# Optimization experiments

Measured on AMD Instinct MI355X. Metric: run time of the kernel, lower is better.

Reference implementation:

```python
import jax, jax.numpy as jnp
import numpy as np
import math

PHI = (1.0 + math.sqrt(5.0)) / 2.0
V, D, L, N, H = 50257, 128, 2, 512, 8
DH = D // H
B, S = 2, 256


def setup_inputs() -> dict:
    key = jax.random.key(0)
    ks = jax.random.split(key, 16)
    lim = 0.5 * math.sqrt(6.0 / (N + D))  # xavier_uniform gain=0.5 for Linear(N->D)
    return {
        "tokens": jax.random.randint(ks[0], (B, S), 0, V),
        "emb": (jax.random.normal(ks[1], (V, 2 * D)) * 0.02) * 0.5,
        "wq": jax.random.normal(ks[2], (L, H, DH)) * 0.02,
        "bq": jnp.zeros((L, H, DH)),
        "wk": jax.random.normal(ks[3], (L, H, DH)) * 0.02,
        "bk": jnp.zeros((L, H, DH)),
        "w_out": jax.random.normal(ks[4], (L, D)) * 0.02,
        "b_out": jnp.zeros((L, D)),
        "out_scale": jnp.ones((L, D)) * 0.5,
        "Wf": jax.random.normal(ks[5], (L, N, D)) * 0.02,
        "Bf": jnp.zeros((L, N, D)),
        "proj_real": jax.random.uniform(ks[6], (L, D, N), minval=-lim, maxval=lim),
        "proj_imag": jax.random.uniform(ks[7], (L, D, N), minval=-lim, maxval=lim),
        "attn_scale": jnp.ones((L,)),
        "res_scale": jnp.ones((L,)),
        "out_proj": jax.random.normal(ks[8], (V, D)) * 0.02,
    }


def reference(tokens, emb, wq, bq, wk, bk, w_out, b_out, out_scale, Wf, Bf,
              proj_real, proj_imag, attn_scale, res_scale, out_proj):
    dtype = emb.dtype
    wb = emb[tokens]                      # [B,S,2D] token -> (w, b) pairs
    w_e, b_e = wb[..., :D], wb[..., D:]
    t = jnp.arange(S, dtype=dtype)        # timestep per position

    # Recurrent Euler state evolution: theta = s/(1+|w|) + b + t*PHI ; s' = cos+sin
    def step(s, inp):
        w_t, b_t, tt = inp
        theta = s / (1.0 + jnp.abs(w_t)) + b_t + tt * PHI
        s_new = jnp.cos(theta) + jnp.sin(theta)
        return s_new, s_new

    _, states = jax.lax.scan(
        step, jnp.zeros((B, D), dtype),
        (jnp.moveaxis(w_e, 1, 0), jnp.moveaxis(b_e, 1, 0), t))
    states = jnp.moveaxis(states, 0, 1)   # [B,S,D] cached states

    causal = jnp.tril(jnp.ones((S, S), bool))  # cache includes current state
    t_phi = t * PHI
    scale = math.sqrt(2 * DH)

    x = states
    for l in range(L):
        # --- Euler attention ---
        xh = x.reshape(B, S, H, DH)
        th_q = xh / (1.0 + jnp.abs(wq[l])) + bq[l] + t_phi[None, :, None, None]
        q = jnp.concatenate([jnp.cos(th_q), jnp.sin(th_q)], axis=-1)  # [B,S,H,2DH]
        kh = states.reshape(B, S, H, DH)
        th_k = kh / (1.0 + jnp.abs(wk[l])) + bk[l]
        k = jnp.concatenate([jnp.cos(th_k), jnp.sin(th_k)], axis=-1)
        scores = jnp.einsum('bqhd,bkhd->bhqk', q, k) / scale
        scores = jnp.where(causal[None, None], scores, -jnp.inf)
        wts = jax.nn.softmax(scores, axis=-1)
        # each head attends over full-width cached states; heads are summed
        context = jnp.einsum('bhqk,bkd->bqd', wts, states)
        th_o = context / (1.0 + jnp.abs(w_out[l])) + b_out[l] + t_phi[None, :, None]
        attn_out = out_scale[l] * (jnp.cos(th_o) + jnp.sin(th_o))
        # --- Resonant FFN (per-neuron interference) ---
        th_f = x[:, :, None, :] / (1.0 + jnp.abs(Wf[l])) + Bf[l] + t[None, :, None, None]
        cos_sum = jnp.cos(th_f).sum(axis=-1)   # [B,S,N]
        sin_sum = jnp.sin(th_f).sum(axis=-1)
        res = cos_sum @ proj_real[l].T + sin_sum @ proj_imag[l].T
        res = jax.nn.silu(res)
        # additive fusion
        x = x + attn_scale[l] * attn_out + res_scale[l] * res

    logits = x @ out_proj.T                # [B,S,V]
    return logits
```

## Files before the change

### kernel.cpp

```cpp
#include <hip/hip_runtime.h>
#include <hip/hip_bf16.h>

using bf16x8 = __attribute__((ext_vector_type(8))) short;
using f32x4  = __attribute__((ext_vector_type(4))) float;

constexpr int cV  = 50257;
constexpr int cVp = 50688;
constexpr int cD  = 128;
constexpr int cN  = 512;
constexpr int cS  = 256;

#define PHI_F    1.6180339887498949f
#define INV2PI_F 0.15915494309189535f
#define SQRT2_F  1.4142135623730951f

__device__ __forceinline__ float fract1(float x) { return x - floorf(x); }

#if __has_builtin(__builtin_amdgcn_sinf)
__device__ __forceinline__ float sin_rev(float r) { return __builtin_amdgcn_sinf(r); }
__device__ __forceinline__ float cos_rev(float r) { return __builtin_amdgcn_cosf(r); }
#else
__device__ __forceinline__ float sin_rev(float r) { return __sinf(r * 6.2831853071795865f); }
__device__ __forceinline__ float cos_rev(float r) { return __cosf(r * 6.2831853071795865f); }
#endif

__device__ __forceinline__ unsigned short f2bf(float f) {
  unsigned u = __float_as_uint(f);
  unsigned r = (u + 0x7FFFu + ((u >> 16) & 1u)) >> 16;
  return (unsigned short)r;
}

__global__ void k_setup(const int* __restrict__ tokens, const float* __restrict__ emb,
                        float2* __restrict__ mc,
                        const float* __restrict__ pr, const float* __restrict__ pi,
                        float* __restrict__ pTR, float* __restrict__ pTI,
                        const float* __restrict__ W, unsigned short* __restrict__ Wbf) {
  int blk = blockIdx.x;
  if (blk < 256) {
    int idx = blk * 256 + threadIdx.x;
    int t = idx & 255, s = idx >> 8;
    int b = t >> 7, d = t & 127;
    int tok = tokens[b * cS + s];
    float w  = emb[tok * (2 * cD) + d];
    float be = emb[tok * (2 * cD) + cD + d];
    float m2 = SQRT2_F * INV2PI_F / (1.f + fabsf(w));
    float c  = fmaf((float)s, PHI_F, be) * INV2PI_F + 0.125f;
    mc[idx] = make_float2(m2, c);
  } else if (blk < 768) {
    int idx = (blk - 256) * 256 + threadIdx.x;
    int l = idx >> 16, rem = idx & 65535;
    int n = rem >> 7, d = rem & 127;
    int src = (l * cD + d) * cN + n;
    pTR[idx] = pr[src];
    pTI[idx] = pi[src];
  } else {
    int idx = (blk - 768) * 256 + threadIdx.x;
    int row = idx >> 4, c0 = (idx & 15) * 8;
    ushort4 o0 = {0,0,0,0}, o1 = {0,0,0,0};
    if (row < cV) {
      float4 w0 = *(const float4*)(W + (size_t)row * cD + c0);
      float4 w1 = *(const float4*)(W + (size_t)row * cD + c0 + 4);
      o0 = { f2bf(w0.x), f2bf(w0.y), f2bf(w0.z), f2bf(w0.w) };
      o1 = { f2bf(w1.x), f2bf(w1.y), f2bf(w1.z), f2bf(w1.w) };
    }
    unsigned short* dst = Wbf + (size_t)row * cD + c0;
    *(ushort4*)dst = o0;
    *(ushort4*)(dst + 4) = o1;
  }
}

__global__ void k_scan(const float2* __restrict__ mc, float* __restrict__ states) {
  int t = threadIdx.x;
  int b = t >> 7, d = t & 127;
  float2 buf[8];
#pragma unroll
  for (int i = 0; i < 8; ++i) buf[i] = mc[i * 256 + t];
  float sv = 0.f;
  float* out = states + (b * cS) * cD + d;
#pragma unroll 8
  for (int s = 0; s < cS; ++s) {
    float2 v = buf[s & 7];
    if (s + 8 < cS) buf[s & 7] = mc[(s + 8) * 256 + t];
    float r = fmaf(sv, v.x, v.y);
    sv = sin_rev(fract1(r));
    out[s * cD] = sv * SQRT2_F;
  }
}

__global__ __launch_bounds__(512) void k_layer(const float* __restrict__ x, const float* __restrict__ states,
                                               const float* __restrict__ wq, const float* __restrict__ bq,
                                               const float* __restrict__ wk, const float* __restrict__ bk,
                                               const float* __restrict__ Wf, const float* __restrict__ Bf,
                                               float* __restrict__ ctx, float* __restrict__ U, float* __restrict__ Vv) {
  int blk = blockIdx.x;
  if (blk < 256) {
    __shared__ __align__(16) float qrow[2][256];
    __shared__ float Psum[2][256];
    __shared__ float redm[2][4], reds[2][4];
    __shared__ float cred[2][256];
    __shared__ __align__(16) float rkl[128], bkl[128];
    int b = blk >> 7, qp = blk & 127;
    int sub = threadIdx.x >> 8;
    int t = threadIdx.x & 255;
    int q = qp * 2 + sub;
    if (threadIdx.x < 128) {
      int hd = threadIdx.x;
      rkl[hd] = INV2PI_F / (1.f + fabsf(wk[hd]));
      bkl[hd] = bk[hd] * INV2PI_F;
    }
    if (t < 128) {
      int hd = t;
      float rq = 1.f / (1.f + fabsf(wq[hd]));
      float thq = fmaf(x[(b * cS + q) * cD + hd], rq, fmaf((float)q, PHI_F, bq[hd])) * INV2PI_F;
      float fq = fract1(thq);
      qrow[sub][hd]       = cos_rev(fq);
      qrow[sub][128 + hd] = sin_rev(fq);
    }
    Psum[sub][t] = 0.f;
    __syncthreads();
    bool act = (t <= q);
    float sc[8];
    const float4* Sr = (const float4*)(states + (b * cS + t) * cD);
#pragma unroll
    for (int h = 0; h < 8; ++h) {
      float sacc = 0.f;
#pragma unroll
      for (int j = 0; j < 4; ++j) {
        float4 sv4 = Sr[h * 4 + j];
        int hd = h * 16 + j * 4;
        float sva[4] = { sv4.x, sv4.y, sv4.z, sv4.w };
#pragma unroll
        for (int c = 0; c < 4; ++c) {
          float f = fract1(fmaf(sva[c], rkl[hd + c], bkl[hd + c]));
          float ck = cos_rev(f), sk = sin_rev(f);
          sacc = fmaf(qrow[sub][hd + c], ck, fmaf(qrow[sub][128 + hd + c], sk, sacc));
        }
      }
      sc[h] = act ? sacc * 0.17677669529663689f : -3.0e38f;
    }
    int wid = t >> 6;
    for (int h = 0; h < 8; ++h) {
      float v = sc[h];
#pragma unroll
      for (int off = 32; off; off >>= 1) v = fmaxf(v, __shfl_xor(v, off, 64));
      if ((t & 63) == 0) redm[sub][wid] = v;
      __syncthreads();
      float m = fmaxf(fmaxf(redm[sub][0], redm[sub][1]), fmaxf(redm[sub][2], redm[sub][3]));
      float p = act ? __expf(sc[h] - m) : 0.f;
      float ps = p;
#pragma unroll
      for (int off = 32; off; off >>= 1) ps += __shfl_xor(ps, off, 64);
      if ((t & 63) == 0) reds[sub][wid] = ps;
      __syncthreads();
      float tot = reds[sub][0] + reds[sub][1] + reds[sub][2] + reds[sub][3];
      Psum[sub][t] += p / tot;
    }
    __syncthreads();
    int d = t & 127, half = t >> 7;
    float acc = 0.f;
    int k0 = half * 128;
    int kend = min(k0 + 128, q + 1);
    for (int kk = k0; kk < kend; ++kk)
      acc = fmaf(Psum[sub][kk], states[(b * cS + kk) * cD + d], acc);
    cred[sub][t] = acc;
    __syncthreads();
    if (half == 0) ctx[(b * cS + q) * cD + d] = cred[sub][t] + cred[sub][t + 128];
  } else {
    int fblk = blk - 256;
    int ns = fblk & 15, tg = fblk >> 4;
    constexpr int P = 130;
    __shared__ __align__(16) float finv[32 * P];
    __shared__ __align__(16) float fb[32 * P];
    __shared__ __align__(16) float xl[32 * 128];
    int t = threadIdx.x;
#pragma unroll
    for (int i = 0; i < 8; ++i) {
      int idx = t + i * 512;
      int rl = idx >> 7, d = idx & 127;
      int g = (ns * 32 + rl) * cD + d;
      finv[rl * P + d] = INV2PI_F / (1.f + fabsf(Wf[g]));
      fb[rl * P + d]   = Bf[g] * INV2PI_F;
      xl[idx] = x[(tg * 32 + rl) * cD + d];
    }
    __syncthreads();
    int nl = t & 31, tli = t >> 5;
#pragma unroll
    for (int p = 0; p < 2; ++p) {
      int tl = p * 16 + tli;
      int T = tg * 32 + tl;
      float srev = (float)(T & 255) * INV2PI_F;
      float uc = 0.f, us = 0.f;
      const float* fi  = finv + nl * P;
      const float* fbp = fb + nl * P;
      const float* xr  = xl + tl * 128;
#pragma unroll 4
      for (int d = 0; d < cD; d += 2) {
        float2 fiv = *(const float2*)(fi + d);
        float2 fbv = *(const float2*)(fbp + d);
        float2 xv  = *(const float2*)(xr + d);
        float f0 = fract1(fmaf(xv.x, fiv.x, fbv.x) + srev);
        float f1 = fract1(fmaf(xv.y, fiv.y, fbv.y) + srev);
        uc += cos_rev(f0);
        us += sin_rev(f0);
        uc += cos_rev(f1);
        us += sin_rev(f1);
      }
      U[T * cN + ns * 32 + nl]  = uc;
      Vv[T * cN + ns * 32 + nl] = us;
    }
  }
}

__global__ __launch_bounds__(512) void k_res(const float* __restrict__ U, const float* __restrict__ Vv,
                                             const float* __restrict__ pTR, const float* __restrict__ pTI,
                                             const float* __restrict__ ctx, const float* __restrict__ x,
                                             const float* __restrict__ w_out, const float* __restrict__ b_out,
                                             const float* __restrict__ out_scale,
                                             const float* __restrict__ attn_scale, const float* __restrict__ res_scale,
                                             int l, float* __restrict__ xout, unsigned short* __restrict__ xbf) {
  int blk = blockIdx.x;
  int t = threadIdx.x;
  __shared__ __align__(16) float uvU[4][512], uvV[4][512];
  __shared__ __align__(16) float4 part[3][4][32];
#pragma unroll
  for (int i = 0; i < 4; ++i) {
    int idx = t + i * 512;
    int tok = idx >> 9, n = idx & 511;
    uvU[tok][n] = U[(blk * 4 + tok) * cN + n];
    uvV[tok][n] = Vv[(blk * 4 + tok) * cN + n];
  }
  __syncthreads();
  int d4 = t & 31, tok = (t >> 5) & 3, nh = t >> 7;
  int T = blk * 4 + tok, s = T & 255;
  float a0 = 0.f, a1 = 0.f, a2 = 0.f, a3 = 0.f;
  const float* prB = pTR + (size_t)(l * cN) * cD + d4 * 4;
  const float* piB = pTI + (size_t)(l * cN) * cD + d4 * 4;
  int n0 = nh * 128;
#pragma unroll 4
  for (int n = n0; n < n0 + 128; ++n) {
    float4 pr = *(const float4*)(prB + n * cD);
    float4 pi = *(const float4*)(piB + n * cD);
    float wr = uvU[tok][n], wi = uvV[tok][n];
    a0 = fmaf(wr, pr.x, fmaf(wi, pi.x, a0));
    a1 = fmaf(wr, pr.y, fmaf(wi, pi.y, a1));
    a2 = fmaf(wr, pr.z, fmaf(wi, pi.z, a2));
    a3 = fmaf(wr, pr.w, fmaf(wi, pi.w, a3));
  }
  if (nh > 0) part[nh - 1][tok][d4] = make_float4(a0, a1, a2, a3);
  __syncthreads();
  if (nh == 0) {
    float rr[4] = { a0, a1, a2, a3 };
#pragma unroll
    for (int j = 0; j < 3; ++j) {
      float4 p = part[j][tok][d4];
      rr[0] += p.x; rr[1] += p.y; rr[2] += p.z; rr[3] += p.w;
    }
    int di = d4 * 4;
    float4 cx  = *(const float4*)(ctx + T * cD + di);
    float4 wo  = *(const float4*)(w_out + l * cD + di);
    float4 bo  = *(const float4*)(b_out + l * cD + di);
    float4 osc = *(const float4*)(out_scale + l * cD + di);
    float4 xv  = *(const float4*)(x + T * cD + di);
    float as = attn_scale[l], rs = res_scale[l];
    float sphi = (float)s * PHI_F;
    float cxa[4] = { cx.x, cx.y, cx.z, cx.w };
    float woa[4] = { wo.x, wo.y, wo.z, wo.w };
    float boa[4] = { bo.x, bo.y, bo.z, bo.w };
    float osa[4] = { osc.x, osc.y, osc.z, osc.w };
    float xva[4] = { xv.x, xv.y, xv.z, xv.w };
    float oa[4];
#pragma unroll
    for (int c = 0; c < 4; ++c) {
      float th = fmaf(cxa[c], 1.f / (1.f + fabsf(woa[c])), boa[c]) + sphi;
      float f = fract1(th * INV2PI_F);
      float ao = osa[c] * (cos_rev(f) + sin_rev(f));
      float r = rr[c];
      float sil = r / (1.f + __expf(-r));
      oa[c] = fmaf(as, ao, fmaf(rs, sil, xva[c]));
    }
    *(float4*)(xout + T * cD + di) = make_float4(oa[0], oa[1], oa[2], oa[3]);
    if (xbf) {
      ushort4 b4 = { f2bf(oa[0]), f2bf(oa[1]), f2bf(oa[2]), f2bf(oa[3]) };
      *(ushort4*)(xbf + T * cD + di) = b4;
    }
  }
}

__global__ __launch_bounds__(256) void k_gemm(const unsigned short* __restrict__ Xbf,
                                              const unsigned short* __restrict__ Wbf,
                                              float* __restrict__ out) {
  __shared__ __align__(16) float Cst[4][16 * 132];
  int t = threadIdx.x;
  int mchunk = blockIdx.x / 99, vchunk = blockIdx.x % 99;
  int m0 = mchunk * 64;
  int v0 = vchunk * 512;
  int wid = t >> 6, lane = t & 63, lr = lane & 15, lk = lane >> 4;
  int wv = wid * 128;
  const bf16x8* Xp = (const bf16x8*)Xbf;
  const bf16x8* Wp = (const bf16x8*)Wbf;
  f32x4 acc[4][8];
#pragma unroll
  for (int fm = 0; fm < 4; ++fm)
#pragma unroll
    for (int fv = 0; fv < 8; ++fv) acc[fm][fv] = (f32x4){0.f, 0.f, 0.f, 0.f};
#pragma unroll
  for (int ks = 0; ks < 4; ++ks) {
    bf16x8 a[4];
#pragma unroll
    for (int fm = 0; fm < 4; ++fm)
      a[fm] = Xp[(m0 + fm * 16 + lr) * 16 + ks * 4 + lk];
#pragma unroll
    for (int fv = 0; fv < 8; ++fv) {
      bf16x8 b = Wp[(size_t)(v0 + wv + fv * 16 + lr) * 16 + ks * 4 + lk];
#pragma unroll
      for (int fm = 0; fm < 4; ++fm)
        acc[fm][fv] = __builtin_amdgcn_mfma_f32_16x16x32_bf16(a[fm], b, acc[fm][fv], 0, 0, 0);
    }
  }
  float* Cp = &Cst[wid][0];
  int row2b = lane >> 5;
  int colg  = (lane & 31) * 4;
#pragma unroll
  for (int fm = 0; fm < 4; ++fm) {
#pragma unroll
    for (int fv = 0; fv < 8; ++fv)
#pragma unroll
      for (int r = 0; r < 4; ++r)
        Cp[(lk * 4 + r) * 132 + fv * 16 + lr] = acc[fm][fv][r];
#pragma unroll
    for (int step = 0; step < 8; ++step) {
      int rowl = step * 2 + row2b;
      float4 cv = *(const float4*)&Cp[rowl * 132 + colg];
      size_t rb = (size_t)(m0 + fm * 16 + rowl) * cV;
      int cb = v0 + wv + colg;
      if (cb + 3 < cV) {
        *(float4*)(out + rb + cb) = cv;
      } else {
        float ca[4] = { cv.x, cv.y, cv.z, cv.w };
#pragma unroll
        for (int j = 0; j < 4; ++j)
          if (cb + j < cV) out[rb + cb + j] = ca[j];
      }
    }
  }
}

extern "C" void kernel_launch(void* const* d_in, const int* in_sizes, int n_in,
                              void* d_out, int out_size, void* d_ws, size_t ws_size,
                              hipStream_t stream) {
  const int*   tokens    = (const int*)d_in[0];
  const float* emb       = (const float*)d_in[1];
  const float* wq        = (const float*)d_in[2];
  const float* bq        = (const float*)d_in[3];
  const float* wk        = (const float*)d_in[4];
  const float* bk        = (const float*)d_in[5];
  const float* w_out     = (const float*)d_in[6];
  const float* b_out     = (const float*)d_in[7];
  const float* out_scale = (const float*)d_in[8];
  const float* Wf        = (const float*)d_in[9];
  const float* Bf        = (const float*)d_in[10];
  const float* pr        = (const float*)d_in[11];
  const float* pi        = (const float*)d_in[12];
  const float* attn_s    = (const float*)d_in[13];
  const float* res_s     = (const float*)d_in[14];
  const float* out_proj  = (const float*)d_in[15];
  float* out = (float*)d_out;
  float* ws  = (float*)d_ws;

  float*  states = ws;
  float*  x1     = ws + 65536;
  float*  x2     = ws + 131072;
  float*  ctx    = ws + 196608;
  float2* mc     = (float2*)(ws + 262144);
  float*  U      = ws + 393216;
  float*  Vv     = ws + 655360;
  float*  pTR    = ws + 917504;
  float*  pTI    = ws + 1048576;
  unsigned short* X2bf = (unsigned short*)(ws + 1179648);
  unsigned short* Wbf  = (unsigned short*)(ws + 1212416);

  k_setup<<<768 + (cVp * 16) / 256, 256, 0, stream>>>(tokens, emb, mc, pr, pi, pTR, pTI,
                                                      out_proj, Wbf);
  k_scan<<<1, 256, 0, stream>>>(mc, states);

  const float* xin = states;
  float* xouts[2] = { x1, x2 };
  for (int l = 0; l < 2; ++l) {
    k_layer<<<512, 512, 0, stream>>>(xin, states, wq + l * 128, bq + l * 128,
                                     wk + l * 128, bk + l * 128,
                                     Wf + l * 65536, Bf + l * 65536, ctx, U, Vv);
    k_res<<<128, 512, 0, stream>>>(U, Vv, pTR, pTI, ctx, xin, w_out, b_out, out_scale,
                                   attn_s, res_s, l, xouts[l],
                                   (l == 1) ? X2bf : (unsigned short*)nullptr);
    xin = xouts[l];
  }
  k_gemm<<<8 * 99, 256, 0, stream>>>(X2bf, Wbf, out);
}
```

Measured before the change: 177.4 us.

## Fuse attention, FFN and residual per token; convert out_proj to bf16 inside GEMM

Merges the per-layer attention, resonant FFN and residual kernels into one per-token kernel, so the U/V and ctx intermediates stay in shared memory and launches drop from three to one per layer. The out_proj fp32-to-bf16 conversion pass is removed, and the GEMM now reads fp32 weights and packs them to bf16 in registers. The GEMM operands are swapped so each lane holds four contiguous output columns, and results are written directly with nontemporal stores instead of staging through LDS. In exchange, the FFN phase now runs in only 256 blocks per layer, each recomputing Wf reciprocals for every token pair, and the GEMM reads twice the weight bytes.

```diff
diff --git a/kernel.cpp b/kernel.cpp
--- a/kernel.cpp
+++ b/kernel.cpp
@@ -5,7 +5,6 @@
 using f32x4  = __attribute__((ext_vector_type(4))) float;
 
 constexpr int cV  = 50257;
-constexpr int cVp = 50688;
 constexpr int cD  = 128;
 constexpr int cN  = 512;
 constexpr int cS  = 256;
@@ -24,17 +23,29 @@
 __device__ __forceinline__ float cos_rev(float r) { return __cosf(r * 6.2831853071795865f); }
 #endif
 
+#if __has_builtin(__builtin_amdgcn_rcpf)
+__device__ __forceinline__ float fast_rcp(float x) { return __builtin_amdgcn_rcpf(x); }
+#else
+__device__ __forceinline__ float fast_rcp(float x) { return 1.f / x; }
+#endif
+
 __device__ __forceinline__ unsigned short f2bf(float f) {
   unsigned u = __float_as_uint(f);
   unsigned r = (u + 0x7FFFu + ((u >> 16) & 1u)) >> 16;
   return (unsigned short)r;
 }
 
+__device__ __forceinline__ bf16x8 pack8(float4 a, float4 b) {
+  union { bf16x8 v; unsigned short u[8]; } r;
+  r.u[0] = f2bf(a.x); r.u[1] = f2bf(a.y); r.u[2] = f2bf(a.z); r.u[3] = f2bf(a.w);
+  r.u[4] = f2bf(b.x); r.u[5] = f2bf(b.y); r.u[6] = f2bf(b.z); r.u[7] = f2bf(b.w);
+  return r.v;
+}
+
 __global__ void k_setup(const int* __restrict__ tokens, const float* __restrict__ emb,
                         float2* __restrict__ mc,
                         const float* __restrict__ pr, const float* __restrict__ pi,
-                        float* __restrict__ pTR, float* __restrict__ pTI,
-                        const float* __restrict__ W, unsigned short* __restrict__ Wbf) {
+                        float* __restrict__ pTR, float* __restrict__ pTI) {
   int blk = blockIdx.x;
   if (blk < 256) {
     int idx = blk * 256 + threadIdx.x;
@@ -46,26 +57,13 @@
     float m2 = SQRT2_F * INV2PI_F / (1.f + fabsf(w));
     float c  = fmaf((float)s, PHI_F, be) * INV2PI_F + 0.125f;
     mc[idx] = make_float2(m2, c);
-  } else if (blk < 768) {
+  } else {
     int idx = (blk - 256) * 256 + threadIdx.x;
     int l = idx >> 16, rem = idx & 65535;
     int n = rem >> 7, d = rem & 127;
     int src = (l * cD + d) * cN + n;
     pTR[idx] = pr[src];
     pTI[idx] = pi[src];
-  } else {
-    int idx = (blk - 768) * 256 + threadIdx.x;
-    int row = idx >> 4, c0 = (idx & 15) * 8;
-    ushort4 o0 = {0,0,0,0}, o1 = {0,0,0,0};
-    if (row < cV) {
-      float4 w0 = *(const float4*)(W + (size_t)row * cD + c0);
-      float4 w1 = *(const float4*)(W + (size_t)row * cD + c0 + 4);
-      o0 = { f2bf(w0.x), f2bf(w0.y), f2bf(w0.z), f2bf(w0.w) };
-      o1 = { f2bf(w1.x), f2bf(w1.y), f2bf(w1.z), f2bf(w1.w) };
-    }
-    unsigned short* dst = Wbf + (size_t)row * cD + c0;
-    *(ushort4*)dst = o0;
-    *(ushort4*)(dst + 4) = o1;
   }
 }
 
@@ -87,75 +85,83 @@
   }
 }
 
-__global__ __launch_bounds__(512) void k_layer(const float* __restrict__ x, const float* __restrict__ states,
-                                               const float* __restrict__ wq, const float* __restrict__ bq,
-                                               const float* __restrict__ wk, const float* __restrict__ bk,
-                                               const float* __restrict__ Wf, const float* __restrict__ Bf,
-                                               float* __restrict__ ctx, float* __restrict__ U, float* __restrict__ Vv) {
+__global__ __launch_bounds__(512) void k_tok(const float* __restrict__ x, const float* __restrict__ states,
+                                             const float* __restrict__ wq, const float* __restrict__ bq,
+                                             const float* __restrict__ wk, const float* __restrict__ bk,
+                                             const float* __restrict__ Wf, const float* __restrict__ Bf,
+                                             const float* __restrict__ pTR, const float* __restrict__ pTI,
+                                             const float* __restrict__ w_out, const float* __restrict__ b_out,
+                                             const float* __restrict__ osc_p,
+                                             const float* __restrict__ attn_s, const float* __restrict__ res_s,
+                                             float* __restrict__ xout, unsigned short* __restrict__ xbf) {
+  __shared__ __align__(16) float qrow[2][256];
+  __shared__ __align__(16) float rkl[128], bkl[128];
+  __shared__ float Psum[2][256];
+  __shared__ float redm[2][4], reds[2][4];
+  __shared__ float cred[2][256];
+  __shared__ __align__(16) float xl[2][128];
+  __shared__ __align__(16) float ctxl[2][128];
+  __shared__ float uvU[2][512], uvV[2][512];
+  __shared__ __align__(16) float4 part[2][8][32];
   int blk = blockIdx.x;
-  if (blk < 256) {
-    __shared__ __align__(16) float qrow[2][256];
-    __shared__ float Psum[2][256];
-    __shared__ float redm[2][4], reds[2][4];
-    __shared__ float cred[2][256];
-    __shared__ __align__(16) float rkl[128], bkl[128];
-    int b = blk >> 7, qp = blk & 127;
-    int sub = threadIdx.x >> 8;
-    int t = threadIdx.x & 255;
-    int q = qp * 2 + sub;
-    if (threadIdx.x < 128) {
-      int hd = threadIdx.x;
-      rkl[hd] = INV2PI_F / (1.f + fabsf(wk[hd]));
-      bkl[hd] = bk[hd] * INV2PI_F;
-    }
-    if (t < 128) {
-      int hd = t;
-      float rq = 1.f / (1.f + fabsf(wq[hd]));
-      float thq = fmaf(x[(b * cS + q) * cD + hd], rq, fmaf((float)q, PHI_F, bq[hd])) * INV2PI_F;
-      float fq = fract1(thq);
-      qrow[sub][hd]       = cos_rev(fq);
-      qrow[sub][128 + hd] = sin_rev(fq);
-    }
-    Psum[sub][t] = 0.f;
+  int b = blk >> 7, qp = blk & 127;
+  int tid = threadIdx.x;
+  int sub = tid >> 8, t = tid & 255;
+  int q = qp * 2 + sub;
+  if (tid < 128) {
+    rkl[tid] = INV2PI_F / (1.f + fabsf(wk[tid]));
+    bkl[tid] = bk[tid] * INV2PI_F;
+  }
+  if (t < 128) {
+    float xv = x[(b * cS + q) * cD + t];
+    xl[sub][t] = xv;
+    float rq = 1.f / (1.f + fabsf(wq[t]));
+    float thq = fmaf(xv, rq, fmaf((float)q, PHI_F, bq[t])) * INV2PI_F;
+    float fq = fract1(thq);
+    qrow[sub][t]       = cos_rev(fq);
+    qrow[sub][128 + t] = sin_rev(fq);
+  }
+  Psum[sub][t] = 0.f;
+  __syncthreads();
+  bool act = (t <= q);
+  float sc[8];
+  const float4* Sr = (const float4*)(states + (b * cS + t) * cD);
+#pragma unroll
+  for (int h = 0; h < 8; ++h) {
+    float sacc = 0.f;
+#pragma unroll
+    for (int j = 0; j < 4; ++j) {
+      float4 sv4 = Sr[h * 4 + j];
+      int hd = h * 16 + j * 4;
+      float sva[4] = { sv4.x, sv4.y, sv4.z, sv4.w };
+#pragma unroll
+      for (int c = 0; c < 4; ++c) {
+        float f = fract1(fmaf(sva[c], rkl[hd + c], bkl[hd + c]));
+        float ck = cos_rev(f), sk = sin_rev(f);
+        sacc = fmaf(qrow[sub][hd + c], ck, fmaf(qrow[sub][128 + hd + c], sk, sacc));
+      }
+    }
+    sc[h] = act ? sacc * 0.17677669529663689f : -3.0e38f;
+  }
+  int wid = t >> 6;
+  for (int h = 0; h < 8; ++h) {
+    float v = sc[h];
+#pragma unroll
+    for (int off = 32; off; off >>= 1) v = fmaxf(v, __shfl_xor(v, off, 64));
+    if ((t & 63) == 0) redm[sub][wid] = v;
     __syncthreads();
-    bool act = (t <= q);
-    float sc[8];
-    const float4* Sr = (const float4*)(states + (b * cS + t) * cD);
-#pragma unroll
-    for (int h = 0; h < 8; ++h) {
-      float sacc = 0.f;
-#pragma unroll
-      for (int j = 0; j < 4; ++j) {
-        float4 sv4 = Sr[h * 4 + j];
-        int hd = h * 16 + j * 4;
-        float sva[4] = { sv4.x, sv4.y, sv4.z, sv4.w };
-#pragma unroll
-        for (int c = 0; c < 4; ++c) {
-          float f = fract1(fmaf(sva[c], rkl[hd + c], bkl[hd + c]));
-          float ck = cos_rev(f), sk = sin_rev(f);
-          sacc = fmaf(qrow[sub][hd + c], ck, fmaf(qrow[sub][128 + hd + c], sk, sacc));
-        }
-      }
-      sc[h] = act ? sacc * 0.17677669529663689f : -3.0e38f;
-    }
-    int wid = t >> 6;
-    for (int h = 0; h < 8; ++h) {
-      float v = sc[h];
-#pragma unroll
-      for (int off = 32; off; off >>= 1) v = fmaxf(v, __shfl_xor(v, off, 64));
-      if ((t & 63) == 0) redm[sub][wid] = v;
-      __syncthreads();
-      float m = fmaxf(fmaxf(redm[sub][0], redm[sub][1]), fmaxf(redm[sub][2], redm[sub][3]));
-      float p = act ? __expf(sc[h] - m) : 0.f;
-      float ps = p;
-#pragma unroll
-      for (int off = 32; off; off >>= 1) ps += __shfl_xor(ps, off, 64);
-      if ((t & 63) == 0) reds[sub][wid] = ps;
-      __syncthreads();
-      float tot = reds[sub][0] + reds[sub][1] + reds[sub][2] + reds[sub][3];
-      Psum[sub][t] += p / tot;
-    }
+    float m = fmaxf(fmaxf(redm[sub][0], redm[sub][1]), fmaxf(redm[sub][2], redm[sub][3]));
+    float p = act ? __expf(sc[h] - m) : 0.f;
+    float ps = p;
+#pragma unroll
+    for (int off = 32; off; off >>= 1) ps += __shfl_xor(ps, off, 64);
+    if ((t & 63) == 0) reds[sub][wid] = ps;
     __syncthreads();
+    float tot = reds[sub][0] + reds[sub][1] + reds[sub][2] + reds[sub][3];
+    Psum[sub][t] += p / tot;
+  }
+  __syncthreads();
+  {
     int d = t & 127, half = t >> 7;
     float acc = 0.f;
     int k0 = half * 128;
@@ -164,140 +170,119 @@
       acc = fmaf(Psum[sub][kk], states[(b * cS + kk) * cD + d], acc);
     cred[sub][t] = acc;
     __syncthreads();
-    if (half == 0) ctx[(b * cS + q) * cD + d] = cred[sub][t] + cred[sub][t + 128];
-  } else {
-    int fblk = blk - 256;
-    int ns = fblk & 15, tg = fblk >> 4;
-    constexpr int P = 130;
-    __shared__ __align__(16) float finv[32 * P];
-    __shared__ __align__(16) float fb[32 * P];
-    __shared__ __align__(16) float xl[32 * 128];
-    int t = threadIdx.x;
-#pragma unroll
-    for (int i = 0; i < 8; ++i) {
-      int idx = t + i * 512;
-      int rl = idx >> 7, d = idx & 127;
-      int g = (ns * 32 + rl) * cD + d;
-      finv[rl * P + d] = INV2PI_F / (1.f + fabsf(Wf[g]));
-      fb[rl * P + d]   = Bf[g] * INV2PI_F;
-      xl[idx] = x[(tg * 32 + rl) * cD + d];
-    }
+    if (half == 0) ctxl[sub][d] = cred[sub][t] + cred[sub][t + 128];
+  }
+  {
+    int lane = tid & 63, wv = tid >> 6;
+    int nrow = lane >> 5, dq = lane & 31;
+    float xa0[4], xa1[4];
+#pragma unroll
+    for (int c = 0; c < 4; ++c) {
+      xa0[c] = xl[0][dq * 4 + c] * INV2PI_F;
+      xa1[c] = xl[1][dq * 4 + c] * INV2PI_F;
+    }
+    float srev0 = (float)(qp * 2) * INV2PI_F;
+    float srev1 = (float)(qp * 2 + 1) * INV2PI_F;
+    for (int p = 0; p < 32; ++p) {
+      int n = ((p * 8 + wv) << 1) + nrow;
+      float4 wf = *(const float4*)(Wf + n * cD + dq * 4);
+      float4 bf = *(const float4*)(Bf + n * cD + dq * 4);
+      float wfa[4] = { wf.x, wf.y, wf.z, wf.w };
+      float bfa[4] = { bf.x, bf.y, bf.z, bf.w };
+      float rcp4[4], fb4[4];
+#pragma unroll
+      for (int c = 0; c < 4; ++c) {
+        rcp4[c] = fast_rcp(1.f + fabsf(wfa[c]));
+        fb4[c]  = bfa[c] * INV2PI_F;
+      }
+#pragma unroll
+      for (int tok = 0; tok < 2; ++tok) {
+        float srev = tok ? srev1 : srev0;
+        float uc = 0.f, us = 0.f;
+#pragma unroll
+        for (int c = 0; c < 4; ++c) {
+          float xc = tok ? xa1[c] : xa0[c];
+          float f = fract1(fmaf(xc, rcp4[c], fb4[c] + srev));
+          uc += cos_rev(f);
+          us += sin_rev(f);
+        }
+#pragma unroll
+        for (int off = 16; off; off >>= 1) {
+          uc += __shfl_xor(uc, off, 32);
+          us += __shfl_xor(us, off, 32);
+        }
+        if (dq == 0) { uvU[tok][n] = uc; uvV[tok][n] = us; }
+      }
+    }
+  }
+  __syncthreads();
+  {
+    int r8 = tid & 255;
+    int d4 = r8 & 31, nh = r8 >> 5;
+    float a0 = 0.f, a1 = 0.f, a2 = 0.f, a3 = 0.f;
+    const float* prB = pTR + d4 * 4;
+    const float* piB = pTI + d4 * 4;
+    int n0 = nh * 64;
+#pragma unroll 4
+    for (int n = n0; n < n0 + 64; ++n) {
+      float4 pr = *(const float4*)(prB + n * cD);
+      float4 pi = *(const float4*)(piB + n * cD);
+      float wr = uvU[sub][n], wi = uvV[sub][n];
+      a0 = fmaf(wr, pr.x, fmaf(wi, pi.x, a0));
+      a1 = fmaf(wr, pr.y, fmaf(wi, pi.y, a1));
+      a2 = fmaf(wr, pr.z, fmaf(wi, pi.z, a2));
+      a3 = fmaf(wr, pr.w, fmaf(wi, pi.w, a3));
+    }
+    part[sub][nh][d4] = make_float4(a0, a1, a2, a3);
     __syncthreads();
-    int nl = t & 31, tli = t >> 5;
-#pragma unroll
-    for (int p = 0; p < 2; ++p) {
-      int tl = p * 16 + tli;
-      int T = tg * 32 + tl;
-      float srev = (float)(T & 255) * INV2PI_F;
-      float uc = 0.f, us = 0.f;
-      const float* fi  = finv + nl * P;
-      const float* fbp = fb + nl * P;
-      const float* xr  = xl + tl * 128;
-#pragma unroll 4
-      for (int d = 0; d < cD; d += 2) {
-        float2 fiv = *(const float2*)(fi + d);
-        float2 fbv = *(const float2*)(fbp + d);
-        float2 xv  = *(const float2*)(xr + d);
-        float f0 = fract1(fmaf(xv.x, fiv.x, fbv.x) + srev);
-        float f1 = fract1(fmaf(xv.y, fiv.y, fbv.y) + srev);
-        uc += cos_rev(f0);
-        us += sin_rev(f0);
-        uc += cos_rev(f1);
-        us += sin_rev(f1);
-      }
-      U[T * cN + ns * 32 + nl]  = uc;
-      Vv[T * cN + ns * 32 + nl] = us;
-    }
-  }
-}
-
-__global__ __launch_bounds__(512) void k_res(const float* __restrict__ U, const float* __restrict__ Vv,
-                                             const float* __restrict__ pTR, const float* __restrict__ pTI,
-                                             const float* __restrict__ ctx, const float* __restrict__ x,
-                                             const float* __restrict__ w_out, const float* __restrict__ b_out,
-                                             const float* __restrict__ out_scale,
-                                             const float* __restrict__ attn_scale, const float* __restrict__ res_scale,
-                                             int l, float* __restrict__ xout, unsigned short* __restrict__ xbf) {
-  int blk = blockIdx.x;
-  int t = threadIdx.x;
-  __shared__ __align__(16) float uvU[4][512], uvV[4][512];
-  __shared__ __align__(16) float4 part[3][4][32];
-#pragma unroll
-  for (int i = 0; i < 4; ++i) {
-    int idx = t + i * 512;
-    int tok = idx >> 9, n = idx & 511;
-    uvU[tok][n] = U[(blk * 4 + tok) * cN + n];
-    uvV[tok][n] = Vv[(blk * 4 + tok) * cN + n];
-  }
-  __syncthreads();
-  int d4 = t & 31, tok = (t >> 5) & 3, nh = t >> 7;
-  int T = blk * 4 + tok, s = T & 255;
-  float a0 = 0.f, a1 = 0.f, a2 = 0.f, a3 = 0.f;
-  const float* prB = pTR + (size_t)(l * cN) * cD + d4 * 4;
-  const float* piB = pTI + (size_t)(l * cN) * cD + d4 * 4;
-  int n0 = nh * 128;
-#pragma unroll 4
-  for (int n = n0; n < n0 + 128; ++n) {
-    float4 pr = *(const float4*)(prB + n * cD);
-    float4 pi = *(const float4*)(piB + n * cD);
-    float wr = uvU[tok][n], wi = uvV[tok][n];
-    a0 = fmaf(wr, pr.x, fmaf(wi, pi.x, a0));
-    a1 = fmaf(wr, pr.y, fmaf(wi, pi.y, a1));
-    a2 = fmaf(wr, pr.z, fmaf(wi, pi.z, a2));
-    a3 = fmaf(wr, pr.w, fmaf(wi, pi.w, a3));
-  }
-  if (nh > 0) part[nh - 1][tok][d4] = make_float4(a0, a1, a2, a3);
-  __syncthreads();
-  if (nh == 0) {
-    float rr[4] = { a0, a1, a2, a3 };
-#pragma unroll
-    for (int j = 0; j < 3; ++j) {
-      float4 p = part[j][tok][d4];
-      rr[0] += p.x; rr[1] += p.y; rr[2] += p.z; rr[3] += p.w;
-    }
-    int di = d4 * 4;
-    float4 cx  = *(const float4*)(ctx + T * cD + di);
-    float4 wo  = *(const float4*)(w_out + l * cD + di);
-    float4 bo  = *(const float4*)(b_out + l * cD + di);
-    float4 osc = *(const float4*)(out_scale + l * cD + di);
-    float4 xv  = *(const float4*)(x + T * cD + di);
-    float as = attn_scale[l], rs = res_scale[l];
-    float sphi = (float)s * PHI_F;
-    float cxa[4] = { cx.x, cx.y, cx.z, cx.w };
-    float woa[4] = { wo.x, wo.y, wo.z, wo.w };
-    float boa[4] = { bo.x, bo.y, bo.z, bo.w };
-    float osa[4] = { osc.x, osc.y, osc.z, osc.w };
-    float xva[4] = { xv.x, xv.y, xv.z, xv.w };
-    float oa[4];
-#pragma unroll
-    for (int c = 0; c < 4; ++c) {
-      float th = fmaf(cxa[c], 1.f / (1.f + fabsf(woa[c])), boa[c]) + sphi;
-      float f = fract1(th * INV2PI_F);
-      float ao = osa[c] * (cos_rev(f) + sin_rev(f));
-      float r = rr[c];
-      float sil = r / (1.f + __expf(-r));
-      oa[c] = fmaf(as, ao, fmaf(rs, sil, xva[c]));
-    }
-    *(float4*)(xout + T * cD + di) = make_float4(oa[0], oa[1], oa[2], oa[3]);
-    if (xbf) {
-      ushort4 b4 = { f2bf(oa[0]), f2bf(oa[1]), f2bf(oa[2]), f2bf(oa[3]) };
-      *(ushort4*)(xbf + T * cD + di) = b4;
+    if (nh == 0) {
+      float rr[4] = { 0.f, 0.f, 0.f, 0.f };
+#pragma unroll
+      for (int j = 0; j < 8; ++j) {
+        float4 p = part[sub][j][d4];
+        rr[0] += p.x; rr[1] += p.y; rr[2] += p.z; rr[3] += p.w;
+      }
+      int di = d4 * 4;
+      float4 cx  = *(const float4*)&ctxl[sub][di];
+      float4 wo  = *(const float4*)(w_out + di);
+      float4 bo  = *(const float4*)(b_out + di);
+      float4 os4 = *(const float4*)(osc_p + di);
+      float4 xv  = *(const float4*)&xl[sub][di];
+      float as = attn_s[0], rs = res_s[0];
+      float sphi = (float)q * PHI_F;
+      float cxa[4] = { cx.x, cx.y, cx.z, cx.w };
+      float woa[4] = { wo.x, wo.y, wo.z, wo.w };
+      float boa[4] = { bo.x, bo.y, bo.z, bo.w };
+      float osa[4] = { os4.x, os4.y, os4.z, os4.w };
+      float xva[4] = { xv.x, xv.y, xv.z, xv.w };
+      float oa[4];
+#pragma unroll
+      for (int c = 0; c < 4; ++c) {
+        float th = fmaf(cxa[c], 1.f / (1.f + fabsf(woa[c])), boa[c]) + sphi;
+        float f = fract1(th * INV2PI_F);
+        float ao = osa[c] * (cos_rev(f) + sin_rev(f));
+        float r = rr[c];
+        float sil = r / (1.f + __expf(-r));
+        oa[c] = fmaf(as, ao, fmaf(rs, sil, xva[c]));
+      }
+      *(float4*)(xout + (b * cS + q) * cD + di) = make_float4(oa[0], oa[1], oa[2], oa[3]);
+      if (xbf) {
+        ushort4 b4 = { f2bf(oa[0]), f2bf(oa[1]), f2bf(oa[2]), f2bf(oa[3]) };
+        *(ushort4*)(xbf + (b * cS + q) * cD + di) = b4;
+      }
     }
   }
 }
 
 __global__ __launch_bounds__(256) void k_gemm(const unsigned short* __restrict__ Xbf,
-                                              const unsigned short* __restrict__ Wbf,
+                                              const float* __restrict__ W,
                                               float* __restrict__ out) {
-  __shared__ __align__(16) float Cst[4][16 * 132];
   int t = threadIdx.x;
   int mchunk = blockIdx.x / 99, vchunk = blockIdx.x % 99;
-  int m0 = mchunk * 64;
-  int v0 = vchunk * 512;
+  int m0 = mchunk * 64, v0 = vchunk * 512;
   int wid = t >> 6, lane = t & 63, lr = lane & 15, lk = lane >> 4;
   int wv = wid * 128;
   const bf16x8* Xp = (const bf16x8*)Xbf;
-  const bf16x8* Wp = (const bf16x8*)Wbf;
   f32x4 acc[4][8];
 #pragma unroll
   for (int fm = 0; fm < 4; ++fm)
@@ -305,41 +290,41 @@
     for (int fv = 0; fv < 8; ++fv) acc[fm][fv] = (f32x4){0.f, 0.f, 0.f, 0.f};
 #pragma unroll
   for (int ks = 0; ks < 4; ++ks) {
-    bf16x8 a[4];
+    bf16x8 bX[4];
 #pragma unroll
     for (int fm = 0; fm < 4; ++fm)
-      a[fm] = Xp[(m0 + fm * 16 + lr) * 16 + ks * 4 + lk];
+      bX[fm] = Xp[(m0 + fm * 16 + lr) * 16 + ks * 4 + lk];
 #pragma unroll
     for (int fv = 0; fv < 8; ++fv) {
-      bf16x8 b = Wp[(size_t)(v0 + wv + fv * 16 + lr) * 16 + ks * 4 + lk];
+      int vr = v0 + wv + fv * 16 + lr;
+      bf16x8 aW;
+      if (vr < cV) {
+        const float4* wr4 = (const float4*)(W + (size_t)vr * cD + ks * 32 + lk * 8);
+        aW = pack8(wr4[0], wr4[1]);
+      } else {
+        aW = (bf16x8){0, 0, 0, 0, 0, 0, 0, 0};
+      }
 #pragma unroll
       for (int fm = 0; fm < 4; ++fm)
-        acc[fm][fv] = __builtin_amdgcn_mfma_f32_16x16x32_bf16(a[fm], b, acc[fm][fv], 0, 0, 0);
-    }
-  }
-  float* Cp = &Cst[wid][0];
-  int row2b = lane >> 5;
-  int colg  = (lane & 31) * 4;
+        acc[fm][fv] = __builtin_amdgcn_mfma_f32_16x16x32_bf16(aW, bX[fm], acc[fm][fv], 0, 0, 0);
+    }
+  }
 #pragma unroll
   for (int fm = 0; fm < 4; ++fm) {
-#pragma unroll
-    for (int fv = 0; fv < 8; ++fv)
-#pragma unroll
-      for (int r = 0; r < 4; ++r)
-        Cp[(lk * 4 + r) * 132 + fv * 16 + lr] = acc[fm][fv][r];
-#pragma unroll
-    for (int step = 0; step < 8; ++step) {
-      int rowl = step * 2 + row2b;
-      float4 cv = *(const float4*)&Cp[rowl * 132 + colg];
-      size_t rb = (size_t)(m0 + fm * 16 + rowl) * cV;
-      int cb = v0 + wv + colg;
+    size_t rb = (size_t)(m0 + fm * 16 + lr) * cV;
+#pragma unroll
+    for (int fv = 0; fv < 8; ++fv) {
+      int cb = v0 + wv + fv * 16 + lk * 4;
       if (cb + 3 < cV) {
-        *(float4*)(out + rb + cb) = cv;
+#if __has_builtin(__builtin_nontemporal_store)
+        __builtin_nontemporal_store(acc[fm][fv], (f32x4*)(out + rb + cb));
+#else
+        *(f32x4*)(out + rb + cb) = acc[fm][fv];
+#endif
       } else {
-        float ca[4] = { cv.x, cv.y, cv.z, cv.w };
 #pragma unroll
         for (int j = 0; j < 4; ++j)
-          if (cb + j < cV) out[rb + cb + j] = ca[j];
+          if (cb + j < cV) out[rb + cb + j] = acc[fm][fv][j];
       }
     }
   }
@@ -370,29 +355,25 @@
   float*  states = ws;
   float*  x1     = ws + 65536;
   float*  x2     = ws + 131072;
-  float*  ctx    = ws + 196608;
-  float2* mc     = (float2*)(ws + 262144);
-  float*  U      = ws + 393216;
-  float*  Vv     = ws + 655360;
-  float*  pTR    = ws + 917504;
-  float*  pTI    = ws + 1048576;
-  unsigned short* X2bf = (unsigned short*)(ws + 1179648);
-  unsigned short* Wbf  = (unsigned short*)(ws + 1212416);
-
-  k_setup<<<768 + (cVp * 16) / 256, 256, 0, stream>>>(tokens, emb, mc, pr, pi, pTR, pTI,
-                                                      out_proj, Wbf);
+  float2* mc     = (float2*)(ws + 196608);
+  float*  pTR    = ws + 327680;
+  float*  pTI    = ws + 458752;
+  unsigned short* X2bf = (unsigned short*)(ws + 589824);
+
+  k_setup<<<768, 256, 0, stream>>>(tokens, emb, mc, pr, pi, pTR, pTI);
   k_scan<<<1, 256, 0, stream>>>(mc, states);
 
   const float* xin = states;
   float* xouts[2] = { x1, x2 };
   for (int l = 0; l < 2; ++l) {
-    k_layer<<<512, 512, 0, stream>>>(xin, states, wq + l * 128, bq + l * 128,
-                                     wk + l * 128, bk + l * 128,
-                                     Wf + l * 65536, Bf + l * 65536, ctx, U, Vv);
-    k_res<<<128, 512, 0, stream>>>(U, Vv, pTR, pTI, ctx, xin, w_out, b_out, out_scale,
-                                   attn_s, res_s, l, xouts[l],
-                                   (l == 1) ? X2bf : (unsigned short*)nullptr);
+    k_tok<<<256, 512, 0, stream>>>(xin, states,
+                                   wq + l * 128, bq + l * 128, wk + l * 128, bk + l * 128,
+                                   Wf + l * 65536, Bf + l * 65536,
+                                   pTR + l * 65536, pTI + l * 65536,
+                                   w_out + l * 128, b_out + l * 128, out_scale + l * 128,
+                                   attn_s + l, res_s + l,
+                                   xouts[l], (l == 1) ? X2bf : (unsigned short*)nullptr);
     xin = xouts[l];
   }
-  k_gemm<<<8 * 99, 256, 0, stream>>>(X2bf, Wbf, out);
-}
+  k_gemm<<<8 * 99, 256, 0, stream>>>(X2bf, out_proj, out);
+}
```

New measurement: 269.5 us. 51.9% more time.
